# Kernel optimization log

Hardware: AMD Instinct MI355X
Metric: run time of the kernel (lower is better)

The kernel has to match this reference:

```python
import jax, jax.numpy as jnp
import numpy as np

B, L, E, H = 8, 1024, 1024, 16
A = E // H  # head dim 64
SCALE = A ** -0.5
NEG = jnp.finfo(jnp.float32).min


def setup_inputs() -> dict:
    key = jax.random.key(0)
    k1, k2, k3, k4, k5 = jax.random.split(key, 5)
    embeddings = jax.random.normal(k1, (B, L, E), dtype=jnp.float32)
    attn_mask = jax.random.randint(k2, (B, H, L, L), 0, 2) == 1
    attn_bias = jax.random.normal(k3, (B, H, L, L), dtype=jnp.float32)
    W_qkv = jax.random.normal(k4, (3 * E, E), dtype=jnp.float32) * (E ** -0.5)
    W_out = jax.random.normal(k5, (E, E), dtype=jnp.float32) * (E ** -0.5)
    return {"embeddings": embeddings, "attn_mask": attn_mask,
            "attn_bias": attn_bias, "W_qkv": W_qkv, "W_out": W_out}


def reference(embeddings, attn_mask, attn_bias, W_qkv, W_out):
    # fused QKV projection: torch Linear -> x @ W.T
    qkv = embeddings @ W_qkv.T                      # [B, L, 3E]
    qkv = qkv.reshape(B, L, H, 3 * A).transpose(0, 2, 1, 3)  # [B, H, L, 3A]
    q, k, v = jnp.split(qkv, 3, axis=-1)            # each [B, H, L, A]
    attn = jnp.einsum('bhqa,bhka->bhqk', q, k) * SCALE
    attn = attn + attn_bias
    attn = jnp.where(attn_mask, NEG, attn)
    attn = jax.nn.softmax(attn, axis=-1)
    values = jnp.einsum('bhqk,bhka->bhqa', attn, v)  # [B, H, L, A]
    values = values.transpose(0, 2, 1, 3).reshape(B, L, E)
    return values @ W_out.T
```

## Files before the change

kernel.cpp:

```cpp
#include <hip/hip_runtime.h>
#include <cstdint>
#include <cstddef>


typedef __bf16 bf16;
typedef __attribute__((ext_vector_type(8))) __bf16 bf16x8;
typedef __attribute__((ext_vector_type(2))) __bf16 bf16x2;
typedef __attribute__((ext_vector_type(4))) float f32x4;
typedef __attribute__((ext_vector_type(4))) int i32x4;

#define MFMA_BF16(a, b, c) __builtin_amdgcn_mfma_f32_16x16x32_bf16(a, b, c, 0, 0, 0)

static constexpr float SCALE_ = 0.125f;
static constexpr float NEGF  = -3.4028234663852886e38f;

__device__ __forceinline__ void gload_lds16(const bf16* g, bf16* l) {
  __builtin_amdgcn_global_load_lds((const __attribute__((address_space(1))) void*)g,
                                   (__attribute__((address_space(3))) void*)l,
                                   16, 0, 0);
}

__device__ __forceinline__ bf16x8 cvt8(const float* p) {
  f32x4 a = *(const f32x4*)p;
  f32x4 b = *(const f32x4*)(p + 4);
  bf16x8 r = {(bf16)a[0], (bf16)a[1], (bf16)a[2], (bf16)a[3],
              (bf16)b[0], (bf16)b[1], (bf16)b[2], (bf16)b[3]};
  return r;
}

__global__ __launch_bounds__(256) void k_qkv(const float* __restrict__ X,
                                             const float* __restrict__ W,
                                             bf16* __restrict__ Q,
                                             bf16* __restrict__ Kc,
                                             bf16* __restrict__ Vt) {
  constexpr int K = 1024;
  __shared__ __align__(16) bf16 As[128 * 64];
  __shared__ __align__(16) bf16 Bs[128 * 64];
  const int t = threadIdx.x;
  const int lane = t & 63, w = t >> 6;
  const int wr = w >> 1, wc = w & 1;
  const int li = lane & 15, g = lane >> 4;
  const int m0 = (blockIdx.x & 63) * 128;
  const int n0 = (blockIdx.x >> 6) * 128;

  f32x4 acc[4][4] = {};

  for (int kt = 0; kt < K; kt += 64) {
#pragma unroll
    for (int it = 0; it < 4; ++it) {
      int c = it * 256 + t;
      int row = c >> 3, col = (c & 7) << 3;
      *(bf16x8*)(As + c * 8) = cvt8(X + (size_t)(m0 + row) * K + kt + col);
      *(bf16x8*)(Bs + c * 8) = cvt8(W + (size_t)(n0 + row) * K + kt + col);
    }
    __syncthreads();
#pragma unroll
    for (int kk = 0; kk < 2; ++kk) {
      bf16x8 af[4], bfr[4];
#pragma unroll
      for (int i = 0; i < 4; ++i)
        af[i] = *(const bf16x8*)(As + (wr * 64 + i * 16 + li) * 64 + kk * 32 + g * 8);
#pragma unroll
      for (int j = 0; j < 4; ++j)
        bfr[j] = *(const bf16x8*)(Bs + (wc * 64 + j * 16 + li) * 64 + kk * 32 + g * 8);
#pragma unroll
      for (int i = 0; i < 4; ++i)
#pragma unroll
        for (int j = 0; j < 4; ++j)
          acc[i][j] = MFMA_BF16(af[i], bfr[j], acc[i][j]);
    }
    __syncthreads();
  }

#pragma unroll
  for (int i = 0; i < 4; ++i) {
#pragma unroll
    for (int j = 0; j < 4; ++j) {
      int col = n0 + wc * 64 + j * 16 + li;
      int h = col / 192, r = col % 192;
#pragma unroll
      for (int rg = 0; rg < 4; ++rg) {
        int row = m0 + wr * 64 + i * 16 + g * 4 + rg;
        int b = row >> 10, l = row & 1023;
        bf16 v = (bf16)acc[i][j][rg];
        if (r < 64)
          Q[((size_t)((b * 16 + h) * 1024 + l)) * 64 + r] = v;
        else if (r < 128)
          Kc[((size_t)((b * 16 + h) * 1024 + l)) * 64 + (r - 64)] = v;
        else
          Vt[((size_t)((b * 16 + h) * 64 + (r - 128))) * 1024 + l] = v;
      }
    }
  }
}

__global__ __launch_bounds__(256) void k_attn(const bf16* __restrict__ Q,
                                              const bf16* __restrict__ Kc,
                                              const bf16* __restrict__ Vt,
                                              const float* __restrict__ bias,
                                              const int* __restrict__ mask,
                                              bf16* __restrict__ Vals) {
  __shared__ __align__(16) bf16 Plds[4][2][16][72];
  const int t = threadIdx.x, lane = t & 63, w = t >> 6;
  const int li = lane & 15, g = lane >> 4;
  const int lid = blockIdx.x;
  const int bh = lid & 127;
  const int qt = lid >> 7;
  const int b = bh >> 4, h = bh & 15;
  const int q0 = qt * 64 + w * 16;

  const bf16* Qbase = Q + ((size_t)bh << 10) * 64;
  const bf16* Kbase = Kc + ((size_t)bh << 10) * 64;
  const bf16* Vbase = Vt + ((size_t)bh << 6) * 1024;
  const float* brow = bias + ((size_t)bh << 20) + (size_t)(q0 + li) * 1024 + g * 4;
  const int*   mrow = mask + ((size_t)bh << 20) + (size_t)(q0 + li) * 1024 + g * 4;

  bf16x8 qf[2];
#pragma unroll
  for (int c = 0; c < 2; ++c)
    qf[c] = *(const bf16x8*)(Qbase + (size_t)(q0 + li) * 64 + c * 32 + g * 8);

  f32x4 oacc[4] = {};
  float mrun = NEGF;
  float lrun = 0.f;

  f32x4 b4[4];
  i32x4 m4[4];
#pragma unroll
  for (int kkf = 0; kkf < 4; ++kkf) {
    b4[kkf] = *(const f32x4*)(brow + kkf * 16);
    m4[kkf] = *(const i32x4*)(mrow + kkf * 16);
  }

  for (int kt6 = 0; kt6 < 16; ++kt6) {
    const int kkt = kt6 * 64;
    const int par = kt6 & 1;

    f32x4 c4[4];
#pragma unroll
    for (int kkf = 0; kkf < 4; ++kkf)
#pragma unroll
      for (int rg = 0; rg < 4; ++rg)
        c4[kkf][rg] = m4[kkf][rg] ? NEGF : b4[kkf][rg];

    if (kt6 < 15) {
#pragma unroll
      for (int kkf = 0; kkf < 4; ++kkf) {
        b4[kkf] = *(const f32x4*)(brow + kkt + 64 + kkf * 16);
        m4[kkf] = *(const i32x4*)(mrow + kkt + 64 + kkf * 16);
      }
    }

    f32x4 s[4];
#pragma unroll
    for (int kkf = 0; kkf < 4; ++kkf) {
      f32x4 ss = {0.f, 0.f, 0.f, 0.f};
#pragma unroll
      for (int c = 0; c < 2; ++c) {
        bf16x8 kf = *(const bf16x8*)(Kbase + (size_t)(kkt + kkf * 16 + li) * 64 + c * 32 + g * 8);
        ss = MFMA_BF16(kf, qf[c], ss);
      }
      s[kkf] = ss;
    }

    float tmax = NEGF;
#pragma unroll
    for (int kkf = 0; kkf < 4; ++kkf) {
#pragma unroll
      for (int rg = 0; rg < 4; ++rg) {
        float sv = __builtin_fmaf(s[kkf][rg], SCALE_, c4[kkf][rg]);
        s[kkf][rg] = sv;
        tmax = fmaxf(tmax, sv);
      }
    }
    tmax = fmaxf(tmax, __shfl_xor(tmax, 16));
    tmax = fmaxf(tmax, __shfl_xor(tmax, 32));

    float mnew = fmaxf(mrun, tmax);
    float corr = __expf(mrun - mnew);
    float psum = 0.f;

#pragma unroll
    for (int kkf = 0; kkf < 4; ++kkf) {
      float p0 = __expf(s[kkf][0] - mnew);
      float p1 = __expf(s[kkf][1] - mnew);
      float p2 = __expf(s[kkf][2] - mnew);
      float p3 = __expf(s[kkf][3] - mnew);
      psum += (p0 + p1) + (p2 + p3);
      bf16x2 pa = {(bf16)p0, (bf16)p1};
      bf16x2 pb = {(bf16)p2, (bf16)p3};
      *(bf16x2*)(&Plds[w][par][li][kkf * 16 + g * 4])     = pa;
      *(bf16x2*)(&Plds[w][par][li][kkf * 16 + g * 4 + 2]) = pb;
    }
    psum += __shfl_xor(psum, 16);
    psum += __shfl_xor(psum, 32);
    lrun = lrun * corr + psum;
    mrun = mnew;

    float cq[4];
#pragma unroll
    for (int rg = 0; rg < 4; ++rg) cq[rg] = __shfl(corr, g * 4 + rg);
#pragma unroll
    for (int af = 0; af < 4; ++af)
#pragma unroll
      for (int rg = 0; rg < 4; ++rg) oacc[af][rg] *= cq[rg];

#pragma unroll
    for (int c = 0; c < 2; ++c) {
      bf16x8 pf = *(const bf16x8*)(&Plds[w][par][li][c * 32 + g * 8]);
#pragma unroll
      for (int af = 0; af < 4; ++af) {
        bf16x8 vf = *(const bf16x8*)(Vbase + (size_t)(af * 16 + li) * 1024 + kkt + c * 32 + g * 8);
        oacc[af] = MFMA_BF16(pf, vf, oacc[af]);
      }
    }
  }

  float linv[4];
#pragma unroll
  for (int rg = 0; rg < 4; ++rg) linv[rg] = 1.0f / __shfl(lrun, g * 4 + rg);
#pragma unroll
  for (int af = 0; af < 4; ++af) {
#pragma unroll
    for (int rg = 0; rg < 4; ++rg) {
      int q = q0 + g * 4 + rg;
      int col = h * 64 + af * 16 + li;
      Vals[(((size_t)(b * 1024 + q)) << 10) + col] = (bf16)(oacc[af][rg] * linv[rg]);
    }
  }
}

__global__ __launch_bounds__(256) void k_out(const bf16* __restrict__ X,
                                             const float* __restrict__ W,
                                             float* __restrict__ Out) {
  constexpr int K = 1024;
  __shared__ __align__(16) bf16 As[128 * 64];
  __shared__ __align__(16) bf16 Bs[128 * 64];
  const int t = threadIdx.x;
  const int lane = t & 63, w = t >> 6;
  const int wr = w >> 1, wc = w & 1;
  const int li = lane & 15, g = lane >> 4;
  const int m0 = (blockIdx.x & 63) * 128;
  const int n0 = (blockIdx.x >> 6) * 128;

  f32x4 acc[4][4] = {};

  for (int kt = 0; kt < K; kt += 64) {
#pragma unroll
    for (int it = 0; it < 4; ++it) {
      int c = it * 256 + t;
      int row = c >> 3, col = (c & 7) << 3;
      gload_lds16(X + (size_t)(m0 + row) * K + kt + col, As + c * 8);
      *(bf16x8*)(Bs + c * 8) = cvt8(W + (size_t)(n0 + row) * K + kt + col);
    }
    __syncthreads();
#pragma unroll
    for (int kk = 0; kk < 2; ++kk) {
      bf16x8 af[4], bfr[4];
#pragma unroll
      for (int i = 0; i < 4; ++i)
        af[i] = *(const bf16x8*)(As + (wr * 64 + i * 16 + li) * 64 + kk * 32 + g * 8);
#pragma unroll
      for (int j = 0; j < 4; ++j)
        bfr[j] = *(const bf16x8*)(Bs + (wc * 64 + j * 16 + li) * 64 + kk * 32 + g * 8);
#pragma unroll
      for (int i = 0; i < 4; ++i)
#pragma unroll
        for (int j = 0; j < 4; ++j)
          acc[i][j] = MFMA_BF16(af[i], bfr[j], acc[i][j]);
    }
    __syncthreads();
  }

#pragma unroll
  for (int i = 0; i < 4; ++i) {
#pragma unroll
    for (int j = 0; j < 4; ++j) {
      int col = n0 + wc * 64 + j * 16 + li;
#pragma unroll
      for (int rg = 0; rg < 4; ++rg) {
        int row = m0 + wr * 64 + i * 16 + g * 4 + rg;
        Out[((size_t)row << 10) + col] = acc[i][j][rg];
      }
    }
  }
}

extern "C" void kernel_launch(void* const* d_in, const int* in_sizes, int n_in,
                              void* d_out, int out_size, void* d_ws, size_t ws_size,
                              hipStream_t stream) {
  const float* emb  = (const float*)d_in[0];
  const int*   mask = (const int*)d_in[1];
  const float* bias = (const float*)d_in[2];
  const float* Wqkv = (const float*)d_in[3];
  const float* Wout = (const float*)d_in[4];
  float* out = (float*)d_out;

  const size_t HEADS_ELEMS = (size_t)8 * 16 * 1024 * 64;
  bf16* Q    = (bf16*)d_ws;
  bf16* Kc   = Q + HEADS_ELEMS;
  bf16* Vt   = Kc + HEADS_ELEMS;
  bf16* Vals = Vt + HEADS_ELEMS;

  k_qkv<<<dim3(64 * 24), 256, 0, stream>>>(emb, Wqkv, Q, Kc, Vt);
  k_attn<<<dim3(2048), 256, 0, stream>>>(Q, Kc, Vt, bias, mask, Vals);
  k_out<<<dim3(64 * 8), 256, 0, stream>>>(Vals, Wout, out);
}
```

Before: 529.0 us.

## Precombine bias and mask into bf16 buffer before attention, processed in head chunks

Adds a prep kernel that merges the fp32 attention bias and int mask into one bf16 additive term per element, written to workspace. Attention is run in chunks of heads that fit the workspace and reads this compact buffer instead of bias and mask. The aim is to shrink the attention kernel's per-element loads from 8 bytes to 2. The trade-off is an extra full pass that reads 8 bytes and writes 2, plus bf16 rounding of the bias. The masked value also changes to -1e30.

```diff
diff --git a/kernel.cpp b/kernel.cpp
--- a/kernel.cpp
+++ b/kernel.cpp
@@ -5,6 +5,7 @@
 
 typedef __bf16 bf16;
 typedef __attribute__((ext_vector_type(8))) __bf16 bf16x8;
+typedef __attribute__((ext_vector_type(4))) __bf16 bf16x4;
 typedef __attribute__((ext_vector_type(2))) __bf16 bf16x2;
 typedef __attribute__((ext_vector_type(4))) float f32x4;
 typedef __attribute__((ext_vector_type(4))) int i32x4;
@@ -12,7 +13,7 @@
 #define MFMA_BF16(a, b, c) __builtin_amdgcn_mfma_f32_16x16x32_bf16(a, b, c, 0, 0, 0)
 
 static constexpr float SCALE_ = 0.125f;
-static constexpr float NEGF  = -3.4028234663852886e38f;
+static constexpr float NEGC  = -1.0e30f;
 
 __device__ __forceinline__ void gload_lds16(const bf16* g, bf16* l) {
   __builtin_amdgcn_global_load_lds((const __attribute__((address_space(1))) void*)g,
@@ -26,6 +27,25 @@
   bf16x8 r = {(bf16)a[0], (bf16)a[1], (bf16)a[2], (bf16)a[3],
               (bf16)b[0], (bf16)b[1], (bf16)b[2], (bf16)b[3]};
   return r;
+}
+
+__global__ __launch_bounds__(256) void k_prep(const float* __restrict__ bias,
+                                              const int* __restrict__ mask,
+                                              bf16* __restrict__ C, size_t n) {
+  size_t i = ((size_t)blockIdx.x * 256 + threadIdx.x) * 8;
+  const size_t stride = (size_t)gridDim.x * 256 * 8;
+  for (; i < n; i += stride) {
+    f32x4 b0 = *(const f32x4*)(bias + i);
+    f32x4 b1 = *(const f32x4*)(bias + i + 4);
+    i32x4 m0 = *(const i32x4*)(mask + i);
+    i32x4 m1 = *(const i32x4*)(mask + i + 4);
+    bf16x8 c;
+#pragma unroll
+    for (int j = 0; j < 4; ++j) c[j] = (bf16)(m0[j] ? NEGC : b0[j]);
+#pragma unroll
+    for (int j = 0; j < 4; ++j) c[4 + j] = (bf16)(m1[j] ? NEGC : b1[j]);
+    *(bf16x8*)(C + i) = c;
+  }
 }
 
 __global__ __launch_bounds__(256) void k_qkv(const float* __restrict__ X,
@@ -97,9 +117,140 @@
 __global__ __launch_bounds__(256) void k_attn(const bf16* __restrict__ Q,
                                               const bf16* __restrict__ Kc,
                                               const bf16* __restrict__ Vt,
-                                              const float* __restrict__ bias,
-                                              const int* __restrict__ mask,
-                                              bf16* __restrict__ Vals) {
+                                              const bf16* __restrict__ C,
+                                              bf16* __restrict__ Vals,
+                                              int bh0, int chmask, int chshift) {
+  __shared__ __align__(16) bf16 Plds[4][2][16][72];
+  const int t = threadIdx.x, lane = t & 63, w = t >> 6;
+  const int li = lane & 15, g = lane >> 4;
+  const int lid = blockIdx.x;
+  const int bhl = lid & chmask;
+  const int qt = lid >> chshift;
+  const int bh = bh0 + bhl;
+  const int b = bh >> 4, h = bh & 15;
+  const int q0 = qt * 64 + w * 16;
+
+  const bf16* Qbase = Q + ((size_t)bh << 10) * 64;
+  const bf16* Kbase = Kc + ((size_t)bh << 10) * 64;
+  const bf16* Vbase = Vt + ((size_t)bh << 6) * 1024;
+  const bf16* crow  = C + ((size_t)bhl << 20) + (size_t)(q0 + li) * 1024 + g * 4;
+
+  bf16x8 qf[2];
+#pragma unroll
+  for (int c = 0; c < 2; ++c)
+    qf[c] = *(const bf16x8*)(Qbase + (size_t)(q0 + li) * 64 + c * 32 + g * 8);
+
+  f32x4 oacc[4] = {};
+  float mrun = NEGC;
+  float lrun = 0.f;
+
+  bf16x4 cA[4];
+#pragma unroll
+  for (int kkf = 0; kkf < 4; ++kkf)
+    cA[kkf] = *(const bf16x4*)(crow + kkf * 16);
+
+  for (int kt6 = 0; kt6 < 16; ++kt6) {
+    const int kkt = kt6 * 64;
+    const int par = kt6 & 1;
+    const bool more = (kt6 < 15);
+
+    bf16x4 cN[4];
+    if (more) {
+#pragma unroll
+      for (int kkf = 0; kkf < 4; ++kkf)
+        cN[kkf] = *(const bf16x4*)(crow + kkt + 64 + kkf * 16);
+    }
+
+    f32x4 s[4];
+#pragma unroll
+    for (int kkf = 0; kkf < 4; ++kkf) {
+      f32x4 ss = {0.f, 0.f, 0.f, 0.f};
+#pragma unroll
+      for (int c = 0; c < 2; ++c) {
+        bf16x8 kf = *(const bf16x8*)(Kbase + (size_t)(kkt + kkf * 16 + li) * 64 + c * 32 + g * 8);
+        ss = MFMA_BF16(kf, qf[c], ss);
+      }
+      s[kkf] = ss;
+    }
+
+    float tmax = NEGC;
+#pragma unroll
+    for (int kkf = 0; kkf < 4; ++kkf) {
+#pragma unroll
+      for (int rg = 0; rg < 4; ++rg) {
+        float sv = __builtin_fmaf(s[kkf][rg], SCALE_, (float)cA[kkf][rg]);
+        s[kkf][rg] = sv;
+        tmax = fmaxf(tmax, sv);
+      }
+    }
+    tmax = fmaxf(tmax, __shfl_xor(tmax, 16));
+    tmax = fmaxf(tmax, __shfl_xor(tmax, 32));
+
+    float mnew = fmaxf(mrun, tmax);
+    float corr = __expf(mrun - mnew);
+    float psum = 0.f;
+
+#pragma unroll
+    for (int kkf = 0; kkf < 4; ++kkf) {
+      float p0 = __expf(s[kkf][0] - mnew);
+      float p1 = __expf(s[kkf][1] - mnew);
+      float p2 = __expf(s[kkf][2] - mnew);
+      float p3 = __expf(s[kkf][3] - mnew);
+      psum += (p0 + p1) + (p2 + p3);
+      bf16x2 pa = {(bf16)p0, (bf16)p1};
+      bf16x2 pb = {(bf16)p2, (bf16)p3};
+      *(bf16x2*)(&Plds[w][par][li][kkf * 16 + g * 4])     = pa;
+      *(bf16x2*)(&Plds[w][par][li][kkf * 16 + g * 4 + 2]) = pb;
+    }
+    psum += __shfl_xor(psum, 16);
+    psum += __shfl_xor(psum, 32);
+    lrun = lrun * corr + psum;
+    mrun = mnew;
+
+    float cq[4];
+#pragma unroll
+    for (int rg = 0; rg < 4; ++rg) cq[rg] = __shfl(corr, g * 4 + rg);
+#pragma unroll
+    for (int af = 0; af < 4; ++af)
+#pragma unroll
+      for (int rg = 0; rg < 4; ++rg) oacc[af][rg] *= cq[rg];
+
+#pragma unroll
+    for (int c = 0; c < 2; ++c) {
+      bf16x8 pf = *(const bf16x8*)(&Plds[w][par][li][c * 32 + g * 8]);
+#pragma unroll
+      for (int af = 0; af < 4; ++af) {
+        bf16x8 vf = *(const bf16x8*)(Vbase + (size_t)(af * 16 + li) * 1024 + kkt + c * 32 + g * 8);
+        oacc[af] = MFMA_BF16(pf, vf, oacc[af]);
+      }
+    }
+
+    if (more) {
+#pragma unroll
+      for (int kkf = 0; kkf < 4; ++kkf) cA[kkf] = cN[kkf];
+    }
+  }
+
+  float linv[4];
+#pragma unroll
+  for (int rg = 0; rg < 4; ++rg) linv[rg] = 1.0f / __shfl(lrun, g * 4 + rg);
+#pragma unroll
+  for (int af = 0; af < 4; ++af) {
+#pragma unroll
+    for (int rg = 0; rg < 4; ++rg) {
+      int q = q0 + g * 4 + rg;
+      int col = h * 64 + af * 16 + li;
+      Vals[(((size_t)(b * 1024 + q)) << 10) + col] = (bf16)(oacc[af][rg] * linv[rg]);
+    }
+  }
+}
+
+__global__ __launch_bounds__(256) void k_attn_direct(const bf16* __restrict__ Q,
+                                                     const bf16* __restrict__ Kc,
+                                                     const bf16* __restrict__ Vt,
+                                                     const float* __restrict__ bias,
+                                                     const int* __restrict__ mask,
+                                                     bf16* __restrict__ Vals) {
   __shared__ __align__(16) bf16 Plds[4][2][16][72];
   const int t = threadIdx.x, lane = t & 63, w = t >> 6;
   const int li = lane & 15, g = lane >> 4;
@@ -121,7 +272,7 @@
     qf[c] = *(const bf16x8*)(Qbase + (size_t)(q0 + li) * 64 + c * 32 + g * 8);
 
   f32x4 oacc[4] = {};
-  float mrun = NEGF;
+  float mrun = NEGC;
   float lrun = 0.f;
 
   f32x4 b4[4];
@@ -141,7 +292,7 @@
     for (int kkf = 0; kkf < 4; ++kkf)
 #pragma unroll
       for (int rg = 0; rg < 4; ++rg)
-        c4[kkf][rg] = m4[kkf][rg] ? NEGF : b4[kkf][rg];
+        c4[kkf][rg] = m4[kkf][rg] ? NEGC : b4[kkf][rg];
 
     if (kt6 < 15) {
 #pragma unroll
@@ -163,7 +314,7 @@
       s[kkf] = ss;
     }
 
-    float tmax = NEGF;
+    float tmax = NEGC;
 #pragma unroll
     for (int kkf = 0; kkf < 4; ++kkf) {
 #pragma unroll
@@ -175,11 +326,9 @@
     }
     tmax = fmaxf(tmax, __shfl_xor(tmax, 16));
     tmax = fmaxf(tmax, __shfl_xor(tmax, 32));
-
     float mnew = fmaxf(mrun, tmax);
     float corr = __expf(mrun - mnew);
     float psum = 0.f;
-
 #pragma unroll
     for (int kkf = 0; kkf < 4; ++kkf) {
       float p0 = __expf(s[kkf][0] - mnew);
@@ -301,8 +450,27 @@
   bf16* Kc   = Q + HEADS_ELEMS;
   bf16* Vt   = Kc + HEADS_ELEMS;
   bf16* Vals = Vt + HEADS_ELEMS;
+  const size_t used = 4 * HEADS_ELEMS * sizeof(bf16);
+
+  int CH = 0;
+  for (int c = 128; c >= 8; c >>= 1)
+    if (used + (size_t)c * 2097152 <= ws_size) { CH = c; break; }
 
   k_qkv<<<dim3(64 * 24), 256, 0, stream>>>(emb, Wqkv, Q, Kc, Vt);
-  k_attn<<<dim3(2048), 256, 0, stream>>>(Q, Kc, Vt, bias, mask, Vals);
+
+  if (CH) {
+    bf16* C = (bf16*)((char*)d_ws + used);
+    int chshift = __builtin_ctz((unsigned)CH);
+    for (int bh0 = 0; bh0 < 128; bh0 += CH) {
+      k_prep<<<dim3(2048), 256, 0, stream>>>(bias + ((size_t)bh0 << 20),
+                                             mask + ((size_t)bh0 << 20),
+                                             C, (size_t)CH << 20);
+      k_attn<<<dim3(CH * 16), 256, 0, stream>>>(Q, Kc, Vt, C, Vals,
+                                                bh0, CH - 1, chshift);
+    }
+  } else {
+    k_attn_direct<<<dim3(2048), 256, 0, stream>>>(Q, Kc, Vt, bias, mask, Vals);
+  }
+
   k_out<<<dim3(64 * 8), 256, 0, stream>>>(Vals, Wout, out);
 }
```

After: 739.7 us. 39.8% more time.

## Stage bias/mask as bf16 tiles in LDS via coalesced block-wide loads

Applied to the files above, without the earlier changes.

Instead of each lane loading scattered 16-byte pieces of bias and mask rows straight into registers, the whole block cooperatively loads 64x128 chunks with contiguous per-thread addressing. It folds mask and bias into one bf16 value, writes it to a double-buffered LDS tile, and processes two 64-key subtiles per chunk. The goal is better coalescing and more bytes in flight on the dominant bias/mask HBM stream. The costs are a block-wide barrier per chunk, extra LDS use, a launch bound of 3 blocks per CU, and bf16 rounding of the bias. The mask value also changes to -1e30.

```diff
diff --git a/kernel.cpp b/kernel.cpp
--- a/kernel.cpp
+++ b/kernel.cpp
@@ -5,6 +5,7 @@
 
 typedef __bf16 bf16;
 typedef __attribute__((ext_vector_type(8))) __bf16 bf16x8;
+typedef __attribute__((ext_vector_type(4))) __bf16 bf16x4;
 typedef __attribute__((ext_vector_type(2))) __bf16 bf16x2;
 typedef __attribute__((ext_vector_type(4))) float f32x4;
 typedef __attribute__((ext_vector_type(4))) int i32x4;
@@ -12,7 +13,7 @@
 #define MFMA_BF16(a, b, c) __builtin_amdgcn_mfma_f32_16x16x32_bf16(a, b, c, 0, 0, 0)
 
 static constexpr float SCALE_ = 0.125f;
-static constexpr float NEGF  = -3.4028234663852886e38f;
+static constexpr float NEGC  = -1.0e30f;
 
 __device__ __forceinline__ void gload_lds16(const bf16* g, bf16* l) {
   __builtin_amdgcn_global_load_lds((const __attribute__((address_space(1))) void*)g,
@@ -94,26 +95,27 @@
   }
 }
 
-__global__ __launch_bounds__(256) void k_attn(const bf16* __restrict__ Q,
-                                              const bf16* __restrict__ Kc,
-                                              const bf16* __restrict__ Vt,
-                                              const float* __restrict__ bias,
-                                              const int* __restrict__ mask,
-                                              bf16* __restrict__ Vals) {
+__global__ __launch_bounds__(256, 3) void k_attn(const bf16* __restrict__ Q,
+                                                 const bf16* __restrict__ Kc,
+                                                 const bf16* __restrict__ Vt,
+                                                 const float* __restrict__ bias,
+                                                 const int* __restrict__ mask,
+                                                 bf16* __restrict__ Vals) {
+  __shared__ __align__(16) bf16 Clds[2][64][132];
   __shared__ __align__(16) bf16 Plds[4][2][16][72];
   const int t = threadIdx.x, lane = t & 63, w = t >> 6;
   const int li = lane & 15, g = lane >> 4;
   const int lid = blockIdx.x;
   const int bh = lid & 127;
-  const int qt = lid >> 7;
+  const int qb = lid >> 7;
   const int b = bh >> 4, h = bh & 15;
-  const int q0 = qt * 64 + w * 16;
+  const int q0 = qb * 64 + w * 16;
 
   const bf16* Qbase = Q + ((size_t)bh << 10) * 64;
   const bf16* Kbase = Kc + ((size_t)bh << 10) * 64;
   const bf16* Vbase = Vt + ((size_t)bh << 6) * 1024;
-  const float* brow = bias + ((size_t)bh << 20) + (size_t)(q0 + li) * 1024 + g * 4;
-  const int*   mrow = mask + ((size_t)bh << 20) + (size_t)(q0 + li) * 1024 + g * 4;
+  const float* bbase = bias + ((size_t)bh << 20) + (size_t)qb * 64 * 1024;
+  const int*   mbase = mask + ((size_t)bh << 20) + (size_t)qb * 64 * 1024;
 
   bf16x8 qf[2];
 #pragma unroll
@@ -121,97 +123,107 @@
     qf[c] = *(const bf16x8*)(Qbase + (size_t)(q0 + li) * 64 + c * 32 + g * 8);
 
   f32x4 oacc[4] = {};
-  float mrun = NEGF;
+  float mrun = NEGC;
   float lrun = 0.f;
 
-  f32x4 b4[4];
-  i32x4 m4[4];
-#pragma unroll
-  for (int kkf = 0; kkf < 4; ++kkf) {
-    b4[kkf] = *(const f32x4*)(brow + kkf * 16);
-    m4[kkf] = *(const i32x4*)(mrow + kkf * 16);
-  }
-
-  for (int kt6 = 0; kt6 < 16; ++kt6) {
-    const int kkt = kt6 * 64;
-    const int par = kt6 & 1;
-
-    f32x4 c4[4];
-#pragma unroll
-    for (int kkf = 0; kkf < 4; ++kkf)
-#pragma unroll
-      for (int rg = 0; rg < 4; ++rg)
-        c4[kkf][rg] = m4[kkf][rg] ? NEGF : b4[kkf][rg];
-
-    if (kt6 < 15) {
+  f32x4 breg[8];
+  i32x4 mreg[8];
+#pragma unroll
+  for (int i = 0; i < 8; ++i) {
+    int f = i * 1024 + t * 4, r = f >> 7, kk = f & 127;
+    breg[i] = *(const f32x4*)(bbase + (size_t)r * 1024 + kk);
+    mreg[i] = *(const i32x4*)(mbase + (size_t)r * 1024 + kk);
+  }
+
+  for (int c = 0; c < 8; ++c) {
+    const int par = c & 1;
+
+#pragma unroll
+    for (int i = 0; i < 8; ++i) {
+      int f = i * 1024 + t * 4, r = f >> 7, kk = f & 127;
+      bf16x4 cv = {(bf16)(mreg[i][0] ? NEGC : breg[i][0]),
+                   (bf16)(mreg[i][1] ? NEGC : breg[i][1]),
+                   (bf16)(mreg[i][2] ? NEGC : breg[i][2]),
+                   (bf16)(mreg[i][3] ? NEGC : breg[i][3])};
+      *(bf16x4*)(&Clds[par][r][kk]) = cv;
+    }
+    if (c < 7) {
+#pragma unroll
+      for (int i = 0; i < 8; ++i) {
+        int f = i * 1024 + t * 4, r = f >> 7, kk = f & 127;
+        breg[i] = *(const f32x4*)(bbase + (size_t)r * 1024 + (c + 1) * 128 + kk);
+        mreg[i] = *(const i32x4*)(mbase + (size_t)r * 1024 + (c + 1) * 128 + kk);
+      }
+    }
+    __syncthreads();
+
+#pragma unroll
+    for (int sub = 0; sub < 2; ++sub) {
+      const int kkt = c * 128 + sub * 64;
+
+      f32x4 s[4];
 #pragma unroll
       for (int kkf = 0; kkf < 4; ++kkf) {
-        b4[kkf] = *(const f32x4*)(brow + kkt + 64 + kkf * 16);
-        m4[kkf] = *(const i32x4*)(mrow + kkt + 64 + kkf * 16);
-      }
-    }
-
-    f32x4 s[4];
-#pragma unroll
-    for (int kkf = 0; kkf < 4; ++kkf) {
-      f32x4 ss = {0.f, 0.f, 0.f, 0.f};
-#pragma unroll
-      for (int c = 0; c < 2; ++c) {
-        bf16x8 kf = *(const bf16x8*)(Kbase + (size_t)(kkt + kkf * 16 + li) * 64 + c * 32 + g * 8);
-        ss = MFMA_BF16(kf, qf[c], ss);
-      }
-      s[kkf] = ss;
-    }
-
-    float tmax = NEGF;
-#pragma unroll
-    for (int kkf = 0; kkf < 4; ++kkf) {
-#pragma unroll
-      for (int rg = 0; rg < 4; ++rg) {
-        float sv = __builtin_fmaf(s[kkf][rg], SCALE_, c4[kkf][rg]);
-        s[kkf][rg] = sv;
-        tmax = fmaxf(tmax, sv);
-      }
-    }
-    tmax = fmaxf(tmax, __shfl_xor(tmax, 16));
-    tmax = fmaxf(tmax, __shfl_xor(tmax, 32));
-
-    float mnew = fmaxf(mrun, tmax);
-    float corr = __expf(mrun - mnew);
-    float psum = 0.f;
-
-#pragma unroll
-    for (int kkf = 0; kkf < 4; ++kkf) {
-      float p0 = __expf(s[kkf][0] - mnew);
-      float p1 = __expf(s[kkf][1] - mnew);
-      float p2 = __expf(s[kkf][2] - mnew);
-      float p3 = __expf(s[kkf][3] - mnew);
-      psum += (p0 + p1) + (p2 + p3);
-      bf16x2 pa = {(bf16)p0, (bf16)p1};
-      bf16x2 pb = {(bf16)p2, (bf16)p3};
-      *(bf16x2*)(&Plds[w][par][li][kkf * 16 + g * 4])     = pa;
-      *(bf16x2*)(&Plds[w][par][li][kkf * 16 + g * 4 + 2]) = pb;
-    }
-    psum += __shfl_xor(psum, 16);
-    psum += __shfl_xor(psum, 32);
-    lrun = lrun * corr + psum;
-    mrun = mnew;
-
-    float cq[4];
-#pragma unroll
-    for (int rg = 0; rg < 4; ++rg) cq[rg] = __shfl(corr, g * 4 + rg);
-#pragma unroll
-    for (int af = 0; af < 4; ++af)
-#pragma unroll
-      for (int rg = 0; rg < 4; ++rg) oacc[af][rg] *= cq[rg];
-
-#pragma unroll
-    for (int c = 0; c < 2; ++c) {
-      bf16x8 pf = *(const bf16x8*)(&Plds[w][par][li][c * 32 + g * 8]);
-#pragma unroll
-      for (int af = 0; af < 4; ++af) {
-        bf16x8 vf = *(const bf16x8*)(Vbase + (size_t)(af * 16 + li) * 1024 + kkt + c * 32 + g * 8);
-        oacc[af] = MFMA_BF16(pf, vf, oacc[af]);
+        f32x4 ss = {0.f, 0.f, 0.f, 0.f};
+#pragma unroll
+        for (int cc = 0; cc < 2; ++cc) {
+          bf16x8 kf = *(const bf16x8*)(Kbase + (size_t)(kkt + kkf * 16 + li) * 64 + cc * 32 + g * 8);
+          ss = MFMA_BF16(kf, qf[cc], ss);
+        }
+        s[kkf] = ss;
+      }
+
+      float tmax = NEGC;
+#pragma unroll
+      for (int kkf = 0; kkf < 4; ++kkf) {
+        bf16x4 cf = *(const bf16x4*)(&Clds[par][w * 16 + li][sub * 64 + kkf * 16 + g * 4]);
+#pragma unroll
+        for (int rg = 0; rg < 4; ++rg) {
+          float sv = __builtin_fmaf(s[kkf][rg], SCALE_, (float)cf[rg]);
+          s[kkf][rg] = sv;
+          tmax = fmaxf(tmax, sv);
+        }
+      }
+      tmax = fmaxf(tmax, __shfl_xor(tmax, 16));
+      tmax = fmaxf(tmax, __shfl_xor(tmax, 32));
+
+      float mnew = fmaxf(mrun, tmax);
+      float corr = __expf(mrun - mnew);
+      float psum = 0.f;
+
+#pragma unroll
+      for (int kkf = 0; kkf < 4; ++kkf) {
+        float p0 = __expf(s[kkf][0] - mnew);
+        float p1 = __expf(s[kkf][1] - mnew);
+        float p2 = __expf(s[kkf][2] - mnew);
+        float p3 = __expf(s[kkf][3] - mnew);
+        psum += (p0 + p1) + (p2 + p3);
+        bf16x2 pa = {(bf16)p0, (bf16)p1};
+        bf16x2 pb = {(bf16)p2, (bf16)p3};
+        *(bf16x2*)(&Plds[w][sub][li][kkf * 16 + g * 4])     = pa;
+        *(bf16x2*)(&Plds[w][sub][li][kkf * 16 + g * 4 + 2]) = pb;
+      }
+      psum += __shfl_xor(psum, 16);
+      psum += __shfl_xor(psum, 32);
+      lrun = lrun * corr + psum;
+      mrun = mnew;
+
+      float cq[4];
+#pragma unroll
+      for (int rg = 0; rg < 4; ++rg) cq[rg] = __shfl(corr, g * 4 + rg);
+#pragma unroll
+      for (int af = 0; af < 4; ++af)
+#pragma unroll
+        for (int rg = 0; rg < 4; ++rg) oacc[af][rg] *= cq[rg];
+
+#pragma unroll
+      for (int cc = 0; cc < 2; ++cc) {
+        bf16x8 pf = *(const bf16x8*)(&Plds[w][sub][li][cc * 32 + g * 8]);
+#pragma unroll
+        for (int af = 0; af < 4; ++af) {
+          bf16x8 vf = *(const bf16x8*)(Vbase + (size_t)(af * 16 + li) * 1024 + kkt + cc * 32 + g * 8);
+          oacc[af] = MFMA_BF16(pf, vf, oacc[af]);
+        }
       }
     }
   }
```

New measurement: 673.7 us. 27.4% more time.

## Keep P in registers via permlane swaps and compute transposed PV output

Applied to the files above, without the earlier changes.

Removes the LDS round-trip for the softmax probabilities. P is packed to bf16 with v_cvt_pk_bf16_f32 and reshuffled across lanes with v_permlane32/16_swap so it can feed the MFMA B operand directly. The PV product is computed transposed (V as the A operand), so the correction and normalisation factors are per-lane scalars and no shuffles are needed, and output stores become 8-byte vectors. It also adds a minimum of 4 blocks to the launch bounds, which limits registers per thread. The lane-permutation mapping must exactly match the MFMA operand layout or the results will be wrong.

```diff
diff --git a/kernel.cpp b/kernel.cpp
--- a/kernel.cpp
+++ b/kernel.cpp
@@ -5,7 +5,7 @@
 
 typedef __bf16 bf16;
 typedef __attribute__((ext_vector_type(8))) __bf16 bf16x8;
-typedef __attribute__((ext_vector_type(2))) __bf16 bf16x2;
+typedef __attribute__((ext_vector_type(4))) __bf16 bf16x4;
 typedef __attribute__((ext_vector_type(4))) float f32x4;
 typedef __attribute__((ext_vector_type(4))) int i32x4;
 
@@ -94,13 +94,12 @@
   }
 }
 
-__global__ __launch_bounds__(256) void k_attn(const bf16* __restrict__ Q,
-                                              const bf16* __restrict__ Kc,
-                                              const bf16* __restrict__ Vt,
-                                              const float* __restrict__ bias,
-                                              const int* __restrict__ mask,
-                                              bf16* __restrict__ Vals) {
-  __shared__ __align__(16) bf16 Plds[4][2][16][72];
+__global__ __launch_bounds__(256, 4) void k_attn(const bf16* __restrict__ Q,
+                                                 const bf16* __restrict__ Kc,
+                                                 const bf16* __restrict__ Vt,
+                                                 const float* __restrict__ bias,
+                                                 const int* __restrict__ mask,
+                                                 bf16* __restrict__ Vals) {
   const int t = threadIdx.x, lane = t & 63, w = t >> 6;
   const int li = lane & 15, g = lane >> 4;
   const int lid = blockIdx.x;
@@ -120,7 +119,7 @@
   for (int c = 0; c < 2; ++c)
     qf[c] = *(const bf16x8*)(Qbase + (size_t)(q0 + li) * 64 + c * 32 + g * 8);
 
-  f32x4 oacc[4] = {};
+  f32x4 oaccT[4] = {};
   float mrun = NEGF;
   float lrun = 0.f;
 
@@ -134,7 +133,6 @@
 
   for (int kt6 = 0; kt6 < 16; ++kt6) {
     const int kkt = kt6 * 64;
-    const int par = kt6 & 1;
 
     f32x4 c4[4];
 #pragma unroll
@@ -176,57 +174,71 @@
     tmax = fmaxf(tmax, __shfl_xor(tmax, 16));
     tmax = fmaxf(tmax, __shfl_xor(tmax, 32));
 
-    float mnew = fmaxf(mrun, tmax);
-    float corr = __expf(mrun - mnew);
+    const float mnew = fmaxf(mrun, tmax);
+    const float corr = __expf(mrun - mnew);
     float psum = 0.f;
 
 #pragma unroll
     for (int kkf = 0; kkf < 4; ++kkf) {
-      float p0 = __expf(s[kkf][0] - mnew);
-      float p1 = __expf(s[kkf][1] - mnew);
-      float p2 = __expf(s[kkf][2] - mnew);
-      float p3 = __expf(s[kkf][3] - mnew);
-      psum += (p0 + p1) + (p2 + p3);
-      bf16x2 pa = {(bf16)p0, (bf16)p1};
-      bf16x2 pb = {(bf16)p2, (bf16)p3};
-      *(bf16x2*)(&Plds[w][par][li][kkf * 16 + g * 4])     = pa;
-      *(bf16x2*)(&Plds[w][par][li][kkf * 16 + g * 4 + 2]) = pb;
+#pragma unroll
+      for (int rg = 0; rg < 4; ++rg) {
+        float p = __expf(s[kkf][rg] - mnew);
+        s[kkf][rg] = p;
+        psum += p;
+      }
     }
     psum += __shfl_xor(psum, 16);
     psum += __shfl_xor(psum, 32);
     lrun = lrun * corr + psum;
     mrun = mnew;
 
-    float cq[4];
-#pragma unroll
-    for (int rg = 0; rg < 4; ++rg) cq[rg] = __shfl(corr, g * 4 + rg);
 #pragma unroll
     for (int af = 0; af < 4; ++af)
 #pragma unroll
-      for (int rg = 0; rg < 4; ++rg) oacc[af][rg] *= cq[rg];
-
+      for (int rg = 0; rg < 4; ++rg) oaccT[af][rg] *= corr;
+
+    uint32_t Wp[4][2];
+#pragma unroll
+    for (int kkf = 0; kkf < 4; ++kkf) {
+#pragma unroll
+      for (int hh = 0; hh < 2; ++hh) {
+        uint32_t wpk;
+        asm("v_cvt_pk_bf16_f32 %0, %1, %2"
+            : "=v"(wpk) : "v"(s[kkf][2 * hh]), "v"(s[kkf][2 * hh + 1]));
+        Wp[kkf][hh] = wpk;
+      }
+    }
+    bf16x8 bfrag[2];
 #pragma unroll
     for (int c = 0; c < 2; ++c) {
-      bf16x8 pf = *(const bf16x8*)(&Plds[w][par][li][c * 32 + g * 8]);
+      uint32_t A0 = Wp[2 * c][0], A1 = Wp[2 * c][1];
+      uint32_t B0 = Wp[2 * c + 1][0], B1 = Wp[2 * c + 1][1];
+      asm("v_permlane32_swap_b32 %0, %1" : "+v"(A0), "+v"(B0));
+      asm("v_permlane32_swap_b32 %0, %1" : "+v"(A1), "+v"(B1));
+      asm("v_permlane16_swap_b32 %0, %1" : "+v"(A0), "+v"(B0));
+      asm("v_permlane16_swap_b32 %0, %1" : "+v"(A1), "+v"(B1));
+      union { uint32_t u[4]; bf16x8 v; } bu;
+      bu.u[0] = A0; bu.u[1] = A1; bu.u[2] = B0; bu.u[3] = B1;
+      bfrag[c] = bu.v;
+    }
+
+#pragma unroll
+    for (int c = 0; c < 2; ++c) {
 #pragma unroll
       for (int af = 0; af < 4; ++af) {
         bf16x8 vf = *(const bf16x8*)(Vbase + (size_t)(af * 16 + li) * 1024 + kkt + c * 32 + g * 8);
-        oacc[af] = MFMA_BF16(pf, vf, oacc[af]);
-      }
-    }
-  }
-
-  float linv[4];
-#pragma unroll
-  for (int rg = 0; rg < 4; ++rg) linv[rg] = 1.0f / __shfl(lrun, g * 4 + rg);
+        oaccT[af] = MFMA_BF16(vf, bfrag[c], oaccT[af]);
+      }
+    }
+  }
+
+  const float linv = 1.0f / lrun;
+  const int q = q0 + li;
 #pragma unroll
   for (int af = 0; af < 4; ++af) {
-#pragma unroll
-    for (int rg = 0; rg < 4; ++rg) {
-      int q = q0 + g * 4 + rg;
-      int col = h * 64 + af * 16 + li;
-      Vals[(((size_t)(b * 1024 + q)) << 10) + col] = (bf16)(oacc[af][rg] * linv[rg]);
-    }
+    bf16x4 o = {(bf16)(oaccT[af][0] * linv), (bf16)(oaccT[af][1] * linv),
+                (bf16)(oaccT[af][2] * linv), (bf16)(oaccT[af][3] * linv)};
+    *(bf16x4*)(Vals + (((size_t)(b * 1024 + q)) << 10) + h * 64 + af * 16 + g * 4) = o;
   }
 }
 
```

Result: slower. 543.1 us (+2.7%).
